# Performance work log

Hardware: AMD Instinct MI355X
Metric: run time of the kernel (lower is better)

The kernel has to match this reference:

```python
import jax, jax.numpy as jnp
import numpy as np

N_BITS = 4
QN = -(2 ** (N_BITS - 1))      # -8
QP = 2 ** (N_BITS - 1) - 1     # 7

IN_F, OUT_F, RANK, N_STEPS = 4096, 4096, 8, 10


def ste_qdq(x, scale):
    """LSQ-style quantize-dequantize (forward math of STEFunction, zero_point=0)."""
    v = x / scale
    q = jnp.clip(jnp.round(v), QN, QP)
    return q * scale


def setup_inputs() -> dict:
    key = jax.random.key(0)
    ks = jax.random.split(key, 4)
    x = jax.random.normal(ks[0], (4, 2048, IN_F), dtype=jnp.float32)
    pretrained_weight = jax.random.normal(ks[1], (OUT_F, IN_F), dtype=jnp.float32)
    lora_A = jax.random.normal(ks[2], (RANK, IN_F), dtype=jnp.float32) * 0.01
    lora_B = jnp.zeros((OUT_F, RANK), dtype=jnp.float32)
    weight_scale = jnp.ones((OUT_F,), dtype=jnp.float32) * 0.1
    temporal_scales = jnp.ones((N_STEPS,), dtype=jnp.float32) * 0.1
    bias = jnp.zeros((OUT_F,), dtype=jnp.float32)
    return {
        "x": x,
        "pretrained_weight": pretrained_weight,
        "lora_A": lora_A,
        "lora_B": lora_B,
        "weight_scale": weight_scale,
        "temporal_scales": temporal_scales,
        "bias": bias,
        "current_step": 0,
    }


def reference(x, pretrained_weight, lora_A, lora_B, weight_scale, temporal_scales, bias, current_step):
    # LoRA merge: [O,R] @ [R,I] -> [O,I]
    merged_weight = pretrained_weight + lora_B @ lora_A
    # Per-out-channel weight quant (vectorized over the Python loop in the torch source)
    w_q = ste_qdq(merged_weight, weight_scale[:, None])            # [O, I]
    # Temporal activation quant with scalar scale for the current step
    x_q = ste_qdq(x, temporal_scales[current_step])                # [B, S, I]
    # F.linear: x @ W^T + b
    return jnp.einsum('bsi,oi->bso', x_q, w_q) + bias
```

## Files before the change

### kernel.cpp

```cpp
#include <hip/hip_runtime.h>
#include <stdint.h>

#define IN_F   4096
#define OUT_F  4096
#define M_ROWS 8192
#define RANK   8

typedef int v4i __attribute__((ext_vector_type(4)));

__device__ __forceinline__ int qone(float v, float s) {
    float q = rintf(v / s);
    q = fminf(fmaxf(q, -8.0f), 7.0f);
    return (int)q;
}

__device__ __forceinline__ uint32_t qpack4(float a, float b, float c, float d, float s) {
    uint32_t r =  (uint32_t)(qone(a, s) & 0xFF)
               | ((uint32_t)(qone(b, s) & 0xFF) << 8)
               | ((uint32_t)(qone(c, s) & 0xFF) << 16)
               | ((uint32_t)(qone(d, s) & 0xFF) << 24);
    return r;
}

__global__ void quant_w_k(const float* __restrict__ W,
                          const float* __restrict__ lA,
                          const float* __restrict__ lB,
                          const float* __restrict__ sw,
                          uint32_t* __restrict__ qw) {
    int i = blockIdx.x * blockDim.x + threadIdx.x;
    int o = i >> 10;
    int c = i & 1023;
    float4 w = reinterpret_cast<const float4*>(W)[i];
    const float* bo = lB + o * RANK;
#pragma unroll
    for (int r = 0; r < RANK; ++r) {
        float br = bo[r];
        float4 a = reinterpret_cast<const float4*>(lA)[r * 1024 + c];
        w.x = fmaf(br, a.x, w.x);
        w.y = fmaf(br, a.y, w.y);
        w.z = fmaf(br, a.z, w.z);
        w.w = fmaf(br, a.w, w.w);
    }
    qw[i] = qpack4(w.x, w.y, w.z, w.w, sw[o]);
}

__global__ void quant_x_k(const float* __restrict__ x,
                          const float* __restrict__ ts,
                          const int* __restrict__ step,
                          uint32_t* __restrict__ qx) {
    const float s = ts[step[0]];
    int i = blockIdx.x * blockDim.x + threadIdx.x;
    float4 v = reinterpret_cast<const float4*>(x)[i];
    qx[i] = qpack4(v.x, v.y, v.z, v.w, s);
}

#define BM 128
#define BN 128
#define BK 64
#define LTILE (BM * BK)

__device__ __forceinline__ void gload16(const void* g, void* l) {
    __builtin_amdgcn_global_load_lds(
        (const __attribute__((address_space(1))) void*)g,
        (__attribute__((address_space(3))) void*)l,
        16, 0, 0);
}

__global__ __launch_bounds__(256) void gemm_i8_k(
    const char* __restrict__ qx, const char* __restrict__ qw,
    const float* __restrict__ sw, const float* __restrict__ ts,
    const int* __restrict__ step, const float* __restrict__ bias,
    float* __restrict__ out) {

    __shared__ __attribute__((aligned(16))) char lsA[2][LTILE];
    __shared__ __attribute__((aligned(16))) char lsB[2][LTILE];

    const int t    = threadIdx.x;
    const int lane = t & 63;
    const int wave = t >> 6;
    const int wm   = wave >> 1;
    const int wn   = wave & 1;

    int bid = blockIdx.x;
    int swz = (bid & 7) * 256 + (bid >> 3);
    const int tn = swz & 31;
    const int tm = swz >> 5;

    const int srow  = t >> 2;
    const int sslot = t & 3;

    auto stage = [&](int buf, int kt) {
        const size_t k0 = (size_t)kt * BK;
#pragma unroll
        for (int p = 0; p < 2; ++p) {
            int row = p * 64 + srow;
            int f   = (row ^ (row >> 2)) & 3;
            int cg  = sslot ^ f;
            gload16(qx + (size_t)(tm * BM + row) * IN_F + k0 + cg * 16,
                    &lsA[buf][p * 4096 + t * 16]);
            gload16(qw + (size_t)(tn * BN + row) * IN_F + k0 + cg * 16,
                    &lsB[buf][p * 4096 + t * 16]);
        }
    };

    auto rdA = [&](int buf, int mi) -> v4i {
        int row = wm * 64 + mi * 16 + (lane & 15);
        int kc  = lane >> 4;
        int f   = (row ^ (row >> 2)) & 3;
        return *(const v4i*)&lsA[buf][row * 64 + ((kc ^ f) << 4)];
    };
    auto rdB = [&](int buf, int ni) -> v4i {
        int row = wn * 64 + ni * 16 + (lane & 15);
        int kc  = lane >> 4;
        int f   = (row ^ (row >> 2)) & 3;
        return *(const v4i*)&lsB[buf][row * 64 + ((kc ^ f) << 4)];
    };

    v4i acc[4][4] = {};

    stage(0, 0);
    __syncthreads();

    int cur = 0;
    const int NT = IN_F / BK;
    for (int kt = 0; kt < NT; ++kt) {
        if (kt + 1 < NT) stage(cur ^ 1, kt + 1);

        v4i a[4], b[4];
#pragma unroll
        for (int mi = 0; mi < 4; ++mi) a[mi] = rdA(cur, mi);
#pragma unroll
        for (int ni = 0; ni < 4; ++ni) b[ni] = rdB(cur, ni);

#pragma unroll
        for (int mi = 0; mi < 4; ++mi)
#pragma unroll
            for (int ni = 0; ni < 4; ++ni)
                acc[mi][ni] = __builtin_amdgcn_mfma_i32_16x16x64_i8(
                    a[mi], b[ni], acc[mi][ni], 0, 0, 0);

        __syncthreads();
        cur ^= 1;
    }

    const float s_x = ts[step[0]];
#pragma unroll
    for (int ni = 0; ni < 4; ++ni) {
        int col  = tn * BN + wn * 64 + ni * 16 + (lane & 15);
        float sc = s_x * sw[col];
        float bv = bias[col];
#pragma unroll
        for (int mi = 0; mi < 4; ++mi) {
            int row0 = tm * BM + wm * 64 + mi * 16 + (lane >> 4) * 4;
#pragma unroll
            for (int r = 0; r < 4; ++r) {
                out[(size_t)(row0 + r) * OUT_F + col] =
                    (float)acc[mi][ni][r] * sc + bv;
            }
        }
    }
}

extern "C" void kernel_launch(void* const* d_in, const int* in_sizes, int n_in,
                              void* d_out, int out_size, void* d_ws, size_t ws_size,
                              hipStream_t stream) {
    const float* x    = (const float*)d_in[0];
    const float* W    = (const float*)d_in[1];
    const float* lA   = (const float*)d_in[2];
    const float* lB   = (const float*)d_in[3];
    const float* sw   = (const float*)d_in[4];
    const float* ts   = (const float*)d_in[5];
    const float* bias = (const float*)d_in[6];
    const int*   step = (const int*)d_in[7];
    float* out = (float*)d_out;

    char* qw = (char*)d_ws;
    char* qx = (char*)d_ws + (size_t)OUT_F * IN_F;

    quant_w_k<<<(OUT_F * IN_F / 4) / 256, 256, 0, stream>>>(W, lA, lB, sw, (uint32_t*)qw);
    quant_x_k<<<(M_ROWS * IN_F / 4) / 256, 256, 0, stream>>>(x, ts, step, (uint32_t*)qx);

    gemm_i8_k<<<(M_ROWS / BM) * (OUT_F / BN), 256, 0, stream>>>(
        (const char*)qx, (const char*)qw, sw, ts, step, bias, out);
}
```

Before: 492.1 us.

## Enlarge int8 GEMM tiles to 256x256 with four-stage LDS prefetch pipeline

Reworks the int8 MFMA GEMM into 256x256 block tiles computed by 8 waves, with a 4-deep LDS ring buffer, explicit vmcnt waits, raw barriers, split staging interleaved with MFMA phases, and s_setprio around the math. The quantization kernels now process four float4s per thread and multiply by a precomputed reciprocal scale instead of dividing. The GEMM change targets global-memory latency and per-tile reuse, at the cost of 128KB of LDS per block, which limits occupancy. The reciprocal multiply can round differently from true division at rounding ties.

Result: faster. 425.5 us (-13.5%).

```diff
diff --git a/kernel.cpp b/kernel.cpp
--- a/kernel.cpp
+++ b/kernel.cpp
@@ -8,56 +8,65 @@
 
 typedef int v4i __attribute__((ext_vector_type(4)));
 
-__device__ __forceinline__ int qone(float v, float s) {
-    float q = rintf(v / s);
+__device__ __forceinline__ int qclamp(float v, float inv) {
+    float q = rintf(v * inv);
     q = fminf(fmaxf(q, -8.0f), 7.0f);
     return (int)q;
 }
 
-__device__ __forceinline__ uint32_t qpack4(float a, float b, float c, float d, float s) {
-    uint32_t r =  (uint32_t)(qone(a, s) & 0xFF)
-               | ((uint32_t)(qone(b, s) & 0xFF) << 8)
-               | ((uint32_t)(qone(c, s) & 0xFF) << 16)
-               | ((uint32_t)(qone(d, s) & 0xFF) << 24);
+__device__ __forceinline__ uint32_t qpack4(float4 v, float inv) {
+    uint32_t r =  (uint32_t)(qclamp(v.x, inv) & 0xFF)
+               | ((uint32_t)(qclamp(v.y, inv) & 0xFF) << 8)
+               | ((uint32_t)(qclamp(v.z, inv) & 0xFF) << 16)
+               | ((uint32_t)(qclamp(v.w, inv) & 0xFF) << 24);
     return r;
 }
 
-__global__ void quant_w_k(const float* __restrict__ W,
-                          const float* __restrict__ lA,
-                          const float* __restrict__ lB,
-                          const float* __restrict__ sw,
-                          uint32_t* __restrict__ qw) {
-    int i = blockIdx.x * blockDim.x + threadIdx.x;
-    int o = i >> 10;
-    int c = i & 1023;
-    float4 w = reinterpret_cast<const float4*>(W)[i];
-    const float* bo = lB + o * RANK;
-#pragma unroll
-    for (int r = 0; r < RANK; ++r) {
-        float br = bo[r];
-        float4 a = reinterpret_cast<const float4*>(lA)[r * 1024 + c];
-        w.x = fmaf(br, a.x, w.x);
-        w.y = fmaf(br, a.y, w.y);
-        w.z = fmaf(br, a.z, w.z);
-        w.w = fmaf(br, a.w, w.w);
-    }
-    qw[i] = qpack4(w.x, w.y, w.z, w.w, sw[o]);
-}
-
-__global__ void quant_x_k(const float* __restrict__ x,
-                          const float* __restrict__ ts,
-                          const int* __restrict__ step,
-                          uint32_t* __restrict__ qx) {
-    const float s = ts[step[0]];
-    int i = blockIdx.x * blockDim.x + threadIdx.x;
-    float4 v = reinterpret_cast<const float4*>(x)[i];
-    qx[i] = qpack4(v.x, v.y, v.z, v.w, s);
-}
-
-#define BM 128
-#define BN 128
-#define BK 64
-#define LTILE (BM * BK)
+__global__ __launch_bounds__(256) void quant_w_k(
+    const float* __restrict__ W, const float* __restrict__ lA,
+    const float* __restrict__ lB, const float* __restrict__ sw,
+    uint32_t* __restrict__ qw) {
+    const int t = threadIdx.x;
+    const int o = blockIdx.x;
+    const float inv = 1.0f / sw[o];
+    float br[RANK];
+#pragma unroll
+    for (int r = 0; r < RANK; ++r) br[r] = lB[o * RANK + r];
+    const float4* Wo = (const float4*)(W + (size_t)o * IN_F);
+    const float4* A4 = (const float4*)lA;
+#pragma unroll
+    for (int k = 0; k < 4; ++k) {
+        int i = k * 256 + t;
+        float4 w = Wo[i];
+#pragma unroll
+        for (int r = 0; r < RANK; ++r) {
+            float4 a = A4[r * 1024 + i];
+            w.x = fmaf(br[r], a.x, w.x);
+            w.y = fmaf(br[r], a.y, w.y);
+            w.z = fmaf(br[r], a.z, w.z);
+            w.w = fmaf(br[r], a.w, w.w);
+        }
+        qw[(size_t)o * 1024 + i] = qpack4(w, inv);
+    }
+}
+
+__global__ __launch_bounds__(256) void quant_x_k(
+    const float* __restrict__ x, const float* __restrict__ ts,
+    const int* __restrict__ step, uint32_t* __restrict__ qx) {
+    const float inv = 1.0f / ts[step[0]];
+    const int t = threadIdx.x;
+    const size_t base = (size_t)blockIdx.x * 1024;
+#pragma unroll
+    for (int k = 0; k < 4; ++k) {
+        size_t i = base + k * 256 + t;
+        float4 v = ((const float4*)x)[i];
+        qx[i] = qpack4(v, inv);
+    }
+}
+
+#define BKB 64
+#define NTK (IN_F / BKB)
+#define TILEB (256 * BKB)
 
 __device__ __forceinline__ void gload16(const void* g, void* l) {
     __builtin_amdgcn_global_load_lds(
@@ -66,92 +75,98 @@
         16, 0, 0);
 }
 
-__global__ __launch_bounds__(256) void gemm_i8_k(
+__global__ __launch_bounds__(512, 2) void gemm_i8_k(
     const char* __restrict__ qx, const char* __restrict__ qw,
     const float* __restrict__ sw, const float* __restrict__ ts,
     const int* __restrict__ step, const float* __restrict__ bias,
     float* __restrict__ out) {
 
-    __shared__ __attribute__((aligned(16))) char lsA[2][LTILE];
-    __shared__ __attribute__((aligned(16))) char lsB[2][LTILE];
+    __shared__ __attribute__((aligned(16))) char lsA[4][TILEB];
+    __shared__ __attribute__((aligned(16))) char lsB[4][TILEB];
 
     const int t    = threadIdx.x;
     const int lane = t & 63;
     const int wave = t >> 6;
-    const int wm   = wave >> 1;
-    const int wn   = wave & 1;
+    const int wm   = wave >> 2;
+    const int wn   = wave & 3;
 
     int bid = blockIdx.x;
-    int swz = (bid & 7) * 256 + (bid >> 3);
-    const int tn = swz & 31;
-    const int tm = swz >> 5;
-
-    const int srow  = t >> 2;
-    const int sslot = t & 3;
-
-    auto stage = [&](int buf, int kt) {
-        const size_t k0 = (size_t)kt * BK;
-#pragma unroll
-        for (int p = 0; p < 2; ++p) {
-            int row = p * 64 + srow;
-            int f   = (row ^ (row >> 2)) & 3;
-            int cg  = sslot ^ f;
-            gload16(qx + (size_t)(tm * BM + row) * IN_F + k0 + cg * 16,
-                    &lsA[buf][p * 4096 + t * 16]);
-            gload16(qw + (size_t)(tn * BN + row) * IN_F + k0 + cg * 16,
-                    &lsB[buf][p * 4096 + t * 16]);
-        }
+    int swz = (bid & 7) * 64 + (bid >> 3);
+    const int tn = swz & 15;
+    const int tm = swz >> 4;
+
+    const char* gA = qx + (size_t)tm * 256 * IN_F;
+    const char* gB = qw + (size_t)tn * 256 * IN_F;
+
+    auto stage_j = [&](int bb, int T, int j) {
+        int i   = j * 512 + t;
+        int row = i >> 2;
+        int cg  = (i & 3) ^ ((row >> 1) & 3);
+        size_t goff = (size_t)row * IN_F + T * BKB + cg * 16;
+        gload16(gA + goff, &lsA[bb][i * 16]);
+        gload16(gB + goff, &lsB[bb][i * 16]);
     };
-
-    auto rdA = [&](int buf, int mi) -> v4i {
-        int row = wm * 64 + mi * 16 + (lane & 15);
-        int kc  = lane >> 4;
-        int f   = (row ^ (row >> 2)) & 3;
-        return *(const v4i*)&lsA[buf][row * 64 + ((kc ^ f) << 4)];
+    auto rdA = [&](int bb, int mi) -> v4i {
+        int r  = wm * 128 + mi * 16 + (lane & 15);
+        int pc = (lane >> 4) ^ ((r >> 1) & 3);
+        return *(const v4i*)&lsA[bb][r * BKB + pc * 16];
     };
-    auto rdB = [&](int buf, int ni) -> v4i {
-        int row = wn * 64 + ni * 16 + (lane & 15);
-        int kc  = lane >> 4;
-        int f   = (row ^ (row >> 2)) & 3;
-        return *(const v4i*)&lsB[buf][row * 64 + ((kc ^ f) << 4)];
+    auto rdB = [&](int bb, int ni) -> v4i {
+        int r  = wn * 64 + ni * 16 + (lane & 15);
+        int pc = (lane >> 4) ^ ((r >> 1) & 3);
+        return *(const v4i*)&lsB[bb][r * BKB + pc * 16];
     };
 
-    v4i acc[4][4] = {};
-
-    stage(0, 0);
-    __syncthreads();
-
-    int cur = 0;
-    const int NT = IN_F / BK;
-    for (int kt = 0; kt < NT; ++kt) {
-        if (kt + 1 < NT) stage(cur ^ 1, kt + 1);
-
-        v4i a[4], b[4];
-#pragma unroll
-        for (int mi = 0; mi < 4; ++mi) a[mi] = rdA(cur, mi);
-#pragma unroll
-        for (int ni = 0; ni < 4; ++ni) b[ni] = rdB(cur, ni);
-
+    v4i acc[8][4] = {};
+
+#pragma unroll
+    for (int T0 = 0; T0 < 3; ++T0) { stage_j(T0, T0, 0); stage_j(T0, T0, 1); }
+
+    for (int T = 0; T < NTK; ++T) {
+        const int bb = T & 3;
+        if (T < NTK - 2)       asm volatile("s_waitcnt vmcnt(8)" ::: "memory");
+        else if (T == NTK - 2) asm volatile("s_waitcnt vmcnt(4)" ::: "memory");
+        else                   asm volatile("s_waitcnt vmcnt(0)" ::: "memory");
+        __builtin_amdgcn_s_barrier();
+
+        v4i av[4], bv[4];
+#pragma unroll
+        for (int mi = 0; mi < 4; ++mi) av[mi] = rdA(bb, mi);
+#pragma unroll
+        for (int ni = 0; ni < 4; ++ni) bv[ni] = rdB(bb, ni);
+        if (T + 3 < NTK) stage_j((T + 3) & 3, T + 3, 0);
+        __builtin_amdgcn_s_setprio(1);
 #pragma unroll
         for (int mi = 0; mi < 4; ++mi)
 #pragma unroll
             for (int ni = 0; ni < 4; ++ni)
                 acc[mi][ni] = __builtin_amdgcn_mfma_i32_16x16x64_i8(
-                    a[mi], b[ni], acc[mi][ni], 0, 0, 0);
-
-        __syncthreads();
-        cur ^= 1;
+                    av[mi], bv[ni], acc[mi][ni], 0, 0, 0);
+        __builtin_amdgcn_s_setprio(0);
+
+        v4i aw[4];
+#pragma unroll
+        for (int mi = 0; mi < 4; ++mi) aw[mi] = rdA(bb, mi + 4);
+        if (T + 3 < NTK) stage_j((T + 3) & 3, T + 3, 1);
+        __builtin_amdgcn_s_setprio(1);
+#pragma unroll
+        for (int mi = 0; mi < 4; ++mi)
+#pragma unroll
+            for (int ni = 0; ni < 4; ++ni)
+                acc[mi + 4][ni] = __builtin_amdgcn_mfma_i32_16x16x64_i8(
+                    aw[mi], bv[ni], acc[mi + 4][ni], 0, 0, 0);
+        __builtin_amdgcn_s_setprio(0);
     }
 
     const float s_x = ts[step[0]];
 #pragma unroll
     for (int ni = 0; ni < 4; ++ni) {
-        int col  = tn * BN + wn * 64 + ni * 16 + (lane & 15);
+        int col  = tn * 256 + wn * 64 + ni * 16 + (lane & 15);
         float sc = s_x * sw[col];
         float bv = bias[col];
 #pragma unroll
-        for (int mi = 0; mi < 4; ++mi) {
-            int row0 = tm * BM + wm * 64 + mi * 16 + (lane >> 4) * 4;
+        for (int mi = 0; mi < 8; ++mi) {
+            int row0 = tm * 256 + wm * 128 + mi * 16 + (lane >> 4) * 4;
 #pragma unroll
             for (int r = 0; r < 4; ++r) {
                 out[(size_t)(row0 + r) * OUT_F + col] =
@@ -177,9 +192,9 @@
     char* qw = (char*)d_ws;
     char* qx = (char*)d_ws + (size_t)OUT_F * IN_F;
 
-    quant_w_k<<<(OUT_F * IN_F / 4) / 256, 256, 0, stream>>>(W, lA, lB, sw, (uint32_t*)qw);
-    quant_x_k<<<(M_ROWS * IN_F / 4) / 256, 256, 0, stream>>>(x, ts, step, (uint32_t*)qx);
-
-    gemm_i8_k<<<(M_ROWS / BM) * (OUT_F / BN), 256, 0, stream>>>(
+    quant_w_k<<<OUT_F, 256, 0, stream>>>(W, lA, lB, sw, (uint32_t*)qw);
+    quant_x_k<<<M_ROWS * IN_F / 4096, 256, 0, stream>>>(x, ts, step, (uint32_t*)qx);
+
+    gemm_i8_k<<<(M_ROWS / 256) * (OUT_F / 256), 512, 0, stream>>>(
         (const char*)qx, (const char*)qw, sw, ts, step, bias, out);
 }
```
